# Kernel optimization log

Hardware: AMD Instinct MI355X
Metric: run time of the kernel (lower is better)

Reference implementation:

```python
import jax, jax.numpy as jnp
import numpy as np

DIM = 1024
DIM_QK = 1024
DIM_V = 1024
H = 16
SCALE = 1.0 / (DIM_QK ** 0.5)  # NOTE: module scales by sqrt(dim_qk), not sqrt(head_dim)


def setup_inputs() -> dict:
    key = jax.random.key(0)
    ks = jax.random.split(key, 12)
    B, S = 2, 2048
    q = jax.random.normal(ks[0], (B, S, DIM), jnp.float32)
    k = jax.random.normal(ks[1], (B, S, DIM), jnp.float32)
    v = jax.random.normal(ks[2], (B, S, DIM), jnp.float32)
    mask = jax.random.randint(ks[3], (B, 1, S, S), 0, 2) > 0  # True = masked
    s = 1.0 / np.sqrt(DIM)
    Wq = jax.random.uniform(ks[4], (DIM_QK, DIM), jnp.float32, -s, s)
    bq = jax.random.uniform(ks[5], (DIM_QK,), jnp.float32, -s, s)
    Wk = jax.random.uniform(ks[6], (DIM_QK, DIM), jnp.float32, -s, s)
    bk = jax.random.uniform(ks[7], (DIM_QK,), jnp.float32, -s, s)
    Wv = jax.random.uniform(ks[8], (DIM_V, DIM), jnp.float32, -s, s)
    bv = jax.random.uniform(ks[9], (DIM_V,), jnp.float32, -s, s)
    Wo = jax.random.uniform(ks[10], (DIM_V, DIM), jnp.float32, -s, s)
    bo = jax.random.uniform(ks[11], (DIM_V,), jnp.float32, -s, s)
    return {"q": q, "k": k, "v": v, "mask": mask,
            "Wq": Wq, "bq": bq, "Wk": Wk, "bk": bk,
            "Wv": Wv, "bv": bv, "Wo": Wo, "bo": bo}


def reference(q, k, v, mask, Wq, bq, Wk, bk, Wv, bv, Wo, bo):
    B, Sq, _ = q.shape
    Skv = k.shape[1]
    # projections (torch Linear: x @ W.T + b)
    qh = (q @ Wq.T + bq).reshape(B, Sq, H, DIM_QK // H).transpose(0, 2, 1, 3)   # [B,H,Sq,dk]
    kh = (k @ Wk.T + bk).reshape(B, Skv, H, DIM_QK // H).transpose(0, 2, 1, 3)  # [B,H,Skv,dk]
    vh = (v @ Wv.T + bv).reshape(B, Skv, H, DIM_V // H).transpose(0, 2, 1, 3)   # [B,H,Skv,dv]
    attn = jnp.einsum('bhqd,bhkd->bhqk', qh, kh) * SCALE
    attn = jnp.where(mask, jnp.float32(-1e20), attn)
    attn = jax.nn.softmax(attn, axis=-1)
    # dropout is identity in eval / p=0
    out = jnp.einsum('bhqk,bhkd->bhqd', attn, vh)            # [B,H,Sq,dv]
    out = out.transpose(0, 2, 1, 3).reshape(B, Sq, DIM_V)
    return out @ Wo.T + bo
```

## Files before the change

kernel.cpp:

```cpp
#include <hip/hip_runtime.h>
#include <hip/hip_bf16.h>

typedef __attribute__((ext_vector_type(8))) __bf16 bf16x8;
typedef __attribute__((ext_vector_type(4))) short short4v;
typedef __attribute__((ext_vector_type(4))) float f32x4;
typedef __attribute__((ext_vector_type(4))) unsigned int uint4v;
typedef __attribute__((ext_vector_type(2))) unsigned int uint2v;

#define S_LEN 2048
#define DIM_  1024
#define HDIM  64
#define SCALE2 0.045084441f
#define T_STR 72

#define EXP2F(x) __builtin_amdgcn_exp2f(x)

__device__ __forceinline__ void async_copy16(const void* gp, void* lp) {
  __builtin_amdgcn_global_load_lds(
      (const __attribute__((address_space(1))) unsigned int*)gp,
      (__attribute__((address_space(3))) unsigned int*)lp, 16, 0, 0);
}

__device__ __forceinline__ unsigned f2bf_u(float f) {
  unsigned u = __builtin_bit_cast(unsigned, f);
  return (u + 0x7FFFu + ((u >> 16) & 1u)) >> 16;
}
__device__ __forceinline__ unsigned pack2(float a, float b) {
  return f2bf_u(a) | (f2bf_u(b) << 16);
}
__device__ __forceinline__ unsigned pack2f(float a, float b) {
  unsigned ua = __builtin_bit_cast(unsigned, a) + 0x8000u;
  unsigned ub = __builtin_bit_cast(unsigned, b) + 0x8000u;
  return __builtin_amdgcn_perm(ub, ua, 0x07060302u);
}

__global__ __launch_bounds__(256) void cvt_kernel(
    const float* __restrict__ s0, const float* __restrict__ s1, const float* __restrict__ s2,
    const float* __restrict__ s3, const float* __restrict__ s4, const float* __restrict__ s5,
    const float* __restrict__ s6,
    __hip_bfloat16* __restrict__ d0, __hip_bfloat16* __restrict__ d1, __hip_bfloat16* __restrict__ d2,
    __hip_bfloat16* __restrict__ d3, __hip_bfloat16* __restrict__ d4, __hip_bfloat16* __restrict__ d5,
    __hip_bfloat16* __restrict__ d6)
{
  const float* srcs[7] = {s0, s1, s2, s3, s4, s5, s6};
  __hip_bfloat16* dsts[7] = {d0, d1, d2, d3, d4, d5, d6};
  const int sizes[7] = {4194304, 4194304, 4194304, 1048576, 1048576, 1048576, 1048576};
  int rg = blockIdx.y;
  int base = (blockIdx.x * 256 + threadIdx.x) * 8;
  if (base >= sizes[rg]) return;
  const float* s = srcs[rg] + base;
  f32x4 a = *(const f32x4*)s;
  f32x4 b = *(const f32x4*)(s + 4);
  uint4v o;
  o.x = pack2(a[0], a[1]); o.y = pack2(a[2], a[3]);
  o.z = pack2(b[0], b[1]); o.w = pack2(b[2], b[3]);
  *(uint4v*)(dsts[rg] + base) = o;
}

__global__ __launch_bounds__(256) void maskbits_kernel(
    const int* __restrict__ mask, unsigned long long* __restrict__ bits)
{
  int w = (blockIdx.x * 256 + threadIdx.x) >> 6;
  int lane = threadIdx.x & 63;
  int m = mask[(size_t)w * 64 + lane];
  unsigned long long bal = __ballot(m != 0);
  if (lane == 0) bits[w] = bal;
}

__device__ __forceinline__ void swz(int r, int& m0, int& n0) {
  int g  = r >> 6;
  int yy = (r >> 3) & 7;
  int xl = r & 7;
  m0 = (g * 8 + xl) * 128;
  n0 = yy * 128;
}

__global__ __launch_bounds__(256) void qkv_gemm_kernel(
    const __hip_bfloat16* __restrict__ xq, const __hip_bfloat16* __restrict__ xk,
    const __hip_bfloat16* __restrict__ xv,
    const __hip_bfloat16* __restrict__ Wq, const float* __restrict__ bq,
    const __hip_bfloat16* __restrict__ Wk, const float* __restrict__ bk,
    const __hip_bfloat16* __restrict__ Wv, const float* __restrict__ bv,
    __hip_bfloat16* __restrict__ Q, __hip_bfloat16* __restrict__ Kk,
    __hip_bfloat16* __restrict__ VT)
{
  const __hip_bfloat16 *X, *W; const float* bias;
  if (blockIdx.z == 0)      { X = xq; W = Wq; bias = bq; }
  else if (blockIdx.z == 1) { X = xk; W = Wk; bias = bk; }
  else                      { X = xv; W = Wv; bias = bv; }

  constexpr int K = 1024, N = 1024;
  __shared__ alignas(16) __hip_bfloat16 As[128 * 32];
  __shared__ alignas(16) __hip_bfloat16 Bs[128 * 32];
  const int tid  = threadIdx.x;
  const int lane = tid & 63;
  const int wave = tid >> 6;
  const int t    = lane & 15;
  const int quad = lane >> 4;
  const int wm   = wave >> 1;
  const int wn   = wave & 1;
  int m0, n0;
  swz(blockIdx.x, m0, n0);

  f32x4 acc[4][4] = {};

  for (int k0 = 0; k0 < K; k0 += 32) {
    __syncthreads();
#pragma unroll
    for (int r = 0; r < 2; ++r) {
      int c   = r * 256 + tid;
      int row = c >> 2;
      int col = (c & 3) * 8;
      async_copy16(&X[(size_t)(m0 + row) * K + k0 + col], &As[c * 8]);
      async_copy16(&W[(size_t)(n0 + row) * K + k0 + col], &Bs[c * 8]);
    }
    __syncthreads();
    bf16x8 a[4], b[4];
#pragma unroll
    for (int i = 0; i < 4; ++i)
      a[i] = *(const bf16x8*)&As[(wm * 64 + i * 16 + t) * 32 + quad * 8];
#pragma unroll
    for (int j = 0; j < 4; ++j)
      b[j] = *(const bf16x8*)&Bs[(wn * 64 + j * 16 + t) * 32 + quad * 8];
#pragma unroll
    for (int i = 0; i < 4; ++i)
#pragma unroll
      for (int j = 0; j < 4; ++j)
        acc[i][j] = __builtin_amdgcn_mfma_f32_16x16x32_bf16(a[i], b[j], acc[i][j], 0, 0, 0);
  }

  float bj[4];
#pragma unroll
  for (int j = 0; j < 4; ++j)
    bj[j] = bias[n0 + wn * 64 + j * 16 + t];

  if (blockIdx.z == 2) {
#pragma unroll
    for (int i = 0; i < 4; ++i)
#pragma unroll
      for (int j = 0; j < 4; ++j) {
        int m = m0 + wm * 64 + i * 16 + quad * 4;
        int n = n0 + wn * 64 + j * 16 + t;
        int bb = m >> 11, kv = m & 2047;
        int hh = n >> 6,  dv = n & 63;
        uint2v o;
        o.x = pack2(acc[i][j][0] + bj[j], acc[i][j][1] + bj[j]);
        o.y = pack2(acc[i][j][2] + bj[j], acc[i][j][3] + bj[j]);
        *(uint2v*)&VT[(size_t)(((bb * 16 + hh) * 64) + dv) * 2048 + kv] = o;
      }
  } else {
    const bool isq = (blockIdx.z == 0);
    __hip_bfloat16* Out = isq ? Q : Kk;
    const float sc = isq ? SCALE2 : 1.0f;
#pragma unroll
    for (int i = 0; i < 4; ++i)
#pragma unroll
      for (int j = 0; j < 4; ++j)
#pragma unroll
        for (int r = 0; r < 4; ++r) {
          int m = m0 + wm * 64 + i * 16 + quad * 4 + r;
          int n = n0 + wn * 64 + j * 16 + t;
          Out[(size_t)m * N + n] = __float2bfloat16((acc[i][j][r] + bj[j]) * sc);
        }
  }
}

__global__ __launch_bounds__(256) void proj_gemm_kernel(
    const __hip_bfloat16* __restrict__ X, const __hip_bfloat16* __restrict__ W,
    const float* __restrict__ bias, float* __restrict__ Out)
{
  constexpr int K = 1024, N = 1024;
  __shared__ alignas(16) __hip_bfloat16 As[128 * 32];
  __shared__ alignas(16) __hip_bfloat16 Bs[128 * 32];
  const int tid  = threadIdx.x;
  const int lane = tid & 63;
  const int wave = tid >> 6;
  const int t    = lane & 15;
  const int quad = lane >> 4;
  const int wm   = wave >> 1;
  const int wn   = wave & 1;
  int m0, n0;
  swz(blockIdx.x, m0, n0);

  f32x4 acc[4][4] = {};

  for (int k0 = 0; k0 < K; k0 += 32) {
    __syncthreads();
#pragma unroll
    for (int r = 0; r < 2; ++r) {
      int c   = r * 256 + tid;
      int row = c >> 2;
      int col = (c & 3) * 8;
      async_copy16(&X[(size_t)(m0 + row) * K + k0 + col], &As[c * 8]);
      async_copy16(&W[(size_t)(n0 + row) * K + k0 + col], &Bs[c * 8]);
    }
    __syncthreads();
    bf16x8 a[4], b[4];
#pragma unroll
    for (int i = 0; i < 4; ++i)
      a[i] = *(const bf16x8*)&As[(wm * 64 + i * 16 + t) * 32 + quad * 8];
#pragma unroll
    for (int j = 0; j < 4; ++j)
      b[j] = *(const bf16x8*)&Bs[(wn * 64 + j * 16 + t) * 32 + quad * 8];
#pragma unroll
    for (int i = 0; i < 4; ++i)
#pragma unroll
      for (int j = 0; j < 4; ++j)
        acc[i][j] = __builtin_amdgcn_mfma_f32_16x16x32_bf16(a[i], b[j], acc[i][j], 0, 0, 0);
  }

  float bj[4];
#pragma unroll
  for (int j = 0; j < 4; ++j)
    bj[j] = bias[n0 + wn * 64 + j * 16 + t];
#pragma unroll
  for (int i = 0; i < 4; ++i)
#pragma unroll
    for (int j = 0; j < 4; ++j)
#pragma unroll
      for (int r = 0; r < 4; ++r) {
        int m = m0 + wm * 64 + i * 16 + quad * 4 + r;
        int n = n0 + wn * 64 + j * 16 + t;
        Out[(size_t)m * N + n] = acc[i][j][r] + bj[j];
      }
}

__global__ __launch_bounds__(256) void attn_kernel(
    const __hip_bfloat16* __restrict__ Qb,
    const __hip_bfloat16* __restrict__ Kb,
    const __hip_bfloat16* __restrict__ VT,
    const unsigned long long* __restrict__ mbits,
    __hip_bfloat16* __restrict__ Ob)
{
  const int bid = blockIdx.x;
  const int qt = bid & 31;
  const int h  = (bid >> 5) & 15;
  const int b  = bid >> 9;
  const int qb = qt * 64;

  __shared__ alignas(16) __hip_bfloat16 Qs[64 * T_STR];
  __shared__ alignas(16) __hip_bfloat16 Ks[64 * T_STR];
  __shared__ alignas(16) __hip_bfloat16 Vt[64 * T_STR];

  const int tid  = threadIdx.x;
  const int lane = tid & 63;
  const int wave = tid >> 6;
  const int t    = lane & 15;
  const int quad = lane >> 4;
  const int t7   = t & 7;

#pragma unroll
  for (int r = 0; r < 2; ++r) {
    int c = r * 256 + tid;
    int row = c >> 3, cg = c & 7;
    uint4 raw = *(const uint4*)&Qb[((size_t)(b * S_LEN + qb + row)) * DIM_ + h * HDIM + cg * 8];
    *(uint4*)&Qs[row * T_STR + ((cg ^ (row & 7))) * 8] = raw;
  }
  __syncthreads();

  bf16x8 qf[2];
#pragma unroll
  for (int ks = 0; ks < 2; ++ks)
    qf[ks] = *(const bf16x8*)&Qs[(wave * 16 + t) * T_STR + ((ks * 4 + quad) ^ t7) * 8];

  float lp = 0.f;
  f32x4 o[4] = {};

  const int qg = qb + wave * 16 + t;
  const size_t vtbase = (size_t)((b * 16 + h) * 64) * 2048;
  const size_t mbase = ((size_t)b * S_LEN + qg) * 32;

  for (int kvt = 0; kvt < 32; ++kvt) {
    const int kvb = kvt * 64;
    unsigned long long mw = mbits[mbase + kvt];
    __syncthreads();
#pragma unroll
    for (int r = 0; r < 2; ++r) {
      int c = r * 256 + tid;
      int row = c >> 3, cg = c & 7;
      int sg8 = ((cg ^ (row & 7))) * 8;
      uint4 kraw = *(const uint4*)&Kb[((size_t)(b * S_LEN + kvb + row)) * DIM_ + h * HDIM + cg * 8];
      *(uint4*)&Ks[row * T_STR + sg8] = kraw;
      uint4 vraw = *(const uint4*)&VT[vtbase + (size_t)row * 2048 + kvb + cg * 8];
      *(uint4*)&Vt[row * T_STR + sg8] = vraw;
    }
    __syncthreads();

    f32x4 s4[4];
#pragma unroll
    for (int i = 0; i < 4; ++i) {
      f32x4 z = {};
      bf16x8 a0 = *(const bf16x8*)&Ks[(i * 16 + t) * T_STR + (quad ^ t7) * 8];
      z = __builtin_amdgcn_mfma_f32_16x16x32_bf16(a0, qf[0], z, 0, 0, 0);
      bf16x8 a1 = *(const bf16x8*)&Ks[(i * 16 + t) * T_STR + ((4 + quad) ^ t7) * 8];
      z = __builtin_amdgcn_mfma_f32_16x16x32_bf16(a1, qf[1], z, 0, 0, 0);
      s4[i] = z;
    }

    float e[4][4];
#pragma unroll
    for (int i = 0; i < 4; ++i) {
      unsigned mq = (unsigned)((mw >> (i * 16 + quad * 4)) & 0xFull);
#pragma unroll
      for (int r = 0; r < 4; ++r) {
        float v = ((mq >> r) & 1u) ? -1e20f : s4[i][r];
        float ex = EXP2F(v);
        e[i][r] = ex;
        lp += ex;
      }
    }

    short4v pf[4];
#pragma unroll
    for (int j = 0; j < 4; ++j) {
      uint2v pk;
      pk.x = pack2f(e[j][0], e[j][1]);
      pk.y = pack2f(e[j][2], e[j][3]);
      pf[j] = __builtin_bit_cast(short4v, pk);
    }

#pragma unroll
    for (int j = 0; j < 4; ++j)
#pragma unroll
      for (int n = 0; n < 4; ++n) {
        short4v va = *(const short4v*)&Vt[(n * 16 + t) * T_STR +
                                          (((2 * j + (quad >> 1)) ^ t7) * 8) + (quad & 1) * 4];
        o[n] = __builtin_amdgcn_mfma_f32_16x16x16bf16_1k(va, pf[j], o[n], 0, 0, 0);
      }
  }

  lp += __shfl_xor(lp, 16, 64);
  lp += __shfl_xor(lp, 32, 64);
  float rl = 1.0f / lp;

  __hip_bfloat16* Ts = Qs;
  __syncthreads();
#pragma unroll
  for (int n = 0; n < 4; ++n) {
    uint2v pk;
    pk.x = pack2f(o[n][0] * rl, o[n][1] * rl);
    pk.y = pack2f(o[n][2] * rl, o[n][3] * rl);
    *(uint2v*)&Ts[(wave * 16 + t) * T_STR +
                  (((2 * n + (quad >> 1)) ^ t7) * 8) + (quad & 1) * 4] = pk;
  }
  __syncthreads();
  {
    int row = tid >> 2;
    int g0  = (tid & 3) * 2;
    uint4 x0 = *(const uint4*)&Ts[row * T_STR + ((g0 ^ (row & 7))) * 8];
    uint4 x1 = *(const uint4*)&Ts[row * T_STR + (((g0 + 1) ^ (row & 7))) * 8];
    __hip_bfloat16* dst = &Ob[((size_t)(b * S_LEN + qb + row)) * DIM_ + h * HDIM + g0 * 8];
    *(uint4*)dst = x0;
    *(uint4*)(dst + 8) = x1;
  }
}

extern "C" void kernel_launch(void* const* d_in, const int* in_sizes, int n_in,
                              void* d_out, int out_size, void* d_ws, size_t ws_size,
                              hipStream_t stream) {
  const float* q  = (const float*)d_in[0];
  const float* k  = (const float*)d_in[1];
  const float* v  = (const float*)d_in[2];
  const int*   mk = (const int*)d_in[3];
  const float* Wq = (const float*)d_in[4];
  const float* bq = (const float*)d_in[5];
  const float* Wk = (const float*)d_in[6];
  const float* bk = (const float*)d_in[7];
  const float* Wv = (const float*)d_in[8];
  const float* bv = (const float*)d_in[9];
  const float* Wo = (const float*)d_in[10];
  const float* bo = (const float*)d_in[11];
  float* out = (float*)d_out;

  char* ws = (char*)d_ws;
  const size_t MB = 1024 * 1024;
  __hip_bfloat16* Qb  = (__hip_bfloat16*)(ws);
  __hip_bfloat16* Kb  = (__hip_bfloat16*)(ws + 8  * MB);
  __hip_bfloat16* VTb = (__hip_bfloat16*)(ws + 16 * MB);
  __hip_bfloat16* Ob  = (__hip_bfloat16*)(ws + 24 * MB);
  __hip_bfloat16* xqb = (__hip_bfloat16*)(ws + 32 * MB);
  __hip_bfloat16* xkb = (__hip_bfloat16*)(ws + 40 * MB);
  __hip_bfloat16* xvb = (__hip_bfloat16*)(ws + 48 * MB);
  __hip_bfloat16* Wqb = (__hip_bfloat16*)(ws + 56 * MB);
  __hip_bfloat16* Wkb = (__hip_bfloat16*)(ws + 58 * MB);
  __hip_bfloat16* Wvb = (__hip_bfloat16*)(ws + 60 * MB);
  __hip_bfloat16* Wob = (__hip_bfloat16*)(ws + 62 * MB);
  unsigned long long* mbits = (unsigned long long*)(ws + 64 * MB);

  cvt_kernel<<<dim3(2048, 7), 256, 0, stream>>>(q, k, v, Wq, Wk, Wv, Wo,
                                                xqb, xkb, xvb, Wqb, Wkb, Wvb, Wob);
  maskbits_kernel<<<dim3(32768), 256, 0, stream>>>(mk, mbits);
  qkv_gemm_kernel<<<dim3(256, 1, 3), 256, 0, stream>>>(xqb, xkb, xvb,
                                                       Wqb, bq, Wkb, bk, Wvb, bv,
                                                       Qb, Kb, VTb);
  attn_kernel<<<dim3(1024), 256, 0, stream>>>(Qb, Kb, VTb, mbits, Ob);
  proj_gemm_kernel<<<dim3(256), 256, 0, stream>>>(Ob, Wob, bo, out);
}
```

Baseline: 314.3 us.

## Double KV tile to 128 and replace XOR swizzle with padded LDS strides

The attention kernel now processes 128 keys per iteration instead of 64, which halves the number of loop iterations and barrier pairs. The XOR-swizzled LDS layout is replaced by plain padded row strides (80 for Q/K, 136 for V^T). The aim is to cut synchronisation and address arithmetic overhead. In exchange it uses more LDS and registers per block, which may reduce occupancy, and the padded layout may cause different bank conflicts.

Result: slower. 356.8 us (+13.5%).

```diff
diff --git a/kernel.cpp b/kernel.cpp
--- a/kernel.cpp
+++ b/kernel.cpp
@@ -11,7 +11,8 @@
 #define DIM_  1024
 #define HDIM  64
 #define SCALE2 0.045084441f
-#define T_STR 72
+#define QK_STR 80
+#define VT_STR 136
 
 #define EXP2F(x) __builtin_amdgcn_exp2f(x)
 
@@ -238,30 +239,29 @@
   const int b  = bid >> 9;
   const int qb = qt * 64;
 
-  __shared__ alignas(16) __hip_bfloat16 Qs[64 * T_STR];
-  __shared__ alignas(16) __hip_bfloat16 Ks[64 * T_STR];
-  __shared__ alignas(16) __hip_bfloat16 Vt[64 * T_STR];
+  __shared__ alignas(16) __hip_bfloat16 Qs[64 * QK_STR];
+  __shared__ alignas(16) __hip_bfloat16 Ks[128 * QK_STR];
+  __shared__ alignas(16) __hip_bfloat16 Vt[64 * VT_STR];
 
   const int tid  = threadIdx.x;
   const int lane = tid & 63;
   const int wave = tid >> 6;
   const int t    = lane & 15;
   const int quad = lane >> 4;
-  const int t7   = t & 7;
 
 #pragma unroll
   for (int r = 0; r < 2; ++r) {
     int c = r * 256 + tid;
-    int row = c >> 3, cg = c & 7;
-    uint4 raw = *(const uint4*)&Qb[((size_t)(b * S_LEN + qb + row)) * DIM_ + h * HDIM + cg * 8];
-    *(uint4*)&Qs[row * T_STR + ((cg ^ (row & 7))) * 8] = raw;
+    int row = c >> 3, d0 = (c & 7) * 8;
+    uint4 raw = *(const uint4*)&Qb[((size_t)(b * S_LEN + qb + row)) * DIM_ + h * HDIM + d0];
+    *(uint4*)&Qs[row * QK_STR + d0] = raw;
   }
   __syncthreads();
 
   bf16x8 qf[2];
 #pragma unroll
   for (int ks = 0; ks < 2; ++ks)
-    qf[ks] = *(const bf16x8*)&Qs[(wave * 16 + t) * T_STR + ((ks * 4 + quad) ^ t7) * 8];
+    qf[ks] = *(const bf16x8*)&Qs[(wave * 16 + t) * QK_STR + ks * 32 + quad * 8];
 
   float lp = 0.f;
   f32x4 o[4] = {};
@@ -270,49 +270,49 @@
   const size_t vtbase = (size_t)((b * 16 + h) * 64) * 2048;
   const size_t mbase = ((size_t)b * S_LEN + qg) * 32;
 
-  for (int kvt = 0; kvt < 32; ++kvt) {
-    const int kvb = kvt * 64;
-    unsigned long long mw = mbits[mbase + kvt];
-    __syncthreads();
-#pragma unroll
-    for (int r = 0; r < 2; ++r) {
+  for (int kvt = 0; kvt < 16; ++kvt) {
+    const int kvb = kvt * 128;
+    unsigned long long mw0 = mbits[mbase + kvt * 2];
+    unsigned long long mw1 = mbits[mbase + kvt * 2 + 1];
+    __syncthreads();
+#pragma unroll
+    for (int r = 0; r < 4; ++r) {
       int c = r * 256 + tid;
-      int row = c >> 3, cg = c & 7;
-      int sg8 = ((cg ^ (row & 7))) * 8;
-      uint4 kraw = *(const uint4*)&Kb[((size_t)(b * S_LEN + kvb + row)) * DIM_ + h * HDIM + cg * 8];
-      *(uint4*)&Ks[row * T_STR + sg8] = kraw;
-      uint4 vraw = *(const uint4*)&VT[vtbase + (size_t)row * 2048 + kvb + cg * 8];
-      *(uint4*)&Vt[row * T_STR + sg8] = vraw;
-    }
-    __syncthreads();
-
-    f32x4 s4[4];
-#pragma unroll
-    for (int i = 0; i < 4; ++i) {
+      int row = c >> 3, d0 = (c & 7) * 8;
+      uint4 kraw = *(const uint4*)&Kb[((size_t)(b * S_LEN + kvb + row)) * DIM_ + h * HDIM + d0];
+      *(uint4*)&Ks[row * QK_STR + d0] = kraw;
+    }
+#pragma unroll
+    for (int r = 0; r < 4; ++r) {
+      int c = r * 256 + tid;
+      int row = c >> 4, cg = (c & 15) * 8;
+      uint4 vraw = *(const uint4*)&VT[vtbase + (size_t)row * 2048 + kvb + cg];
+      *(uint4*)&Vt[row * VT_STR + cg] = vraw;
+    }
+    __syncthreads();
+
+    float e[8][4];
+#pragma unroll
+    for (int i = 0; i < 8; ++i) {
       f32x4 z = {};
-      bf16x8 a0 = *(const bf16x8*)&Ks[(i * 16 + t) * T_STR + (quad ^ t7) * 8];
+      bf16x8 a0 = *(const bf16x8*)&Ks[(i * 16 + t) * QK_STR + quad * 8];
       z = __builtin_amdgcn_mfma_f32_16x16x32_bf16(a0, qf[0], z, 0, 0, 0);
-      bf16x8 a1 = *(const bf16x8*)&Ks[(i * 16 + t) * T_STR + ((4 + quad) ^ t7) * 8];
+      bf16x8 a1 = *(const bf16x8*)&Ks[(i * 16 + t) * QK_STR + 32 + quad * 8];
       z = __builtin_amdgcn_mfma_f32_16x16x32_bf16(a1, qf[1], z, 0, 0, 0);
-      s4[i] = z;
-    }
-
-    float e[4][4];
-#pragma unroll
-    for (int i = 0; i < 4; ++i) {
-      unsigned mq = (unsigned)((mw >> (i * 16 + quad * 4)) & 0xFull);
+      unsigned long long mw = (i < 4) ? mw0 : mw1;
+      unsigned mq = (unsigned)((mw >> ((i & 3) * 16 + quad * 4)) & 0xFull);
 #pragma unroll
       for (int r = 0; r < 4; ++r) {
-        float v = ((mq >> r) & 1u) ? -1e20f : s4[i][r];
+        float v = ((mq >> r) & 1u) ? -1e20f : z[r];
         float ex = EXP2F(v);
         e[i][r] = ex;
         lp += ex;
       }
     }
 
-    short4v pf[4];
-#pragma unroll
-    for (int j = 0; j < 4; ++j) {
+    short4v pf[8];
+#pragma unroll
+    for (int j = 0; j < 8; ++j) {
       uint2v pk;
       pk.x = pack2f(e[j][0], e[j][1]);
       pk.y = pack2f(e[j][2], e[j][3]);
@@ -320,11 +320,10 @@
     }
 
 #pragma unroll
-    for (int j = 0; j < 4; ++j)
+    for (int j = 0; j < 8; ++j)
 #pragma unroll
       for (int n = 0; n < 4; ++n) {
-        short4v va = *(const short4v*)&Vt[(n * 16 + t) * T_STR +
-                                          (((2 * j + (quad >> 1)) ^ t7) * 8) + (quad & 1) * 4];
+        short4v va = *(const short4v*)&Vt[(n * 16 + t) * VT_STR + j * 16 + quad * 4];
         o[n] = __builtin_amdgcn_mfma_f32_16x16x16bf16_1k(va, pf[j], o[n], 0, 0, 0);
       }
   }
@@ -340,16 +339,15 @@
     uint2v pk;
     pk.x = pack2f(o[n][0] * rl, o[n][1] * rl);
     pk.y = pack2f(o[n][2] * rl, o[n][3] * rl);
-    *(uint2v*)&Ts[(wave * 16 + t) * T_STR +
-                  (((2 * n + (quad >> 1)) ^ t7) * 8) + (quad & 1) * 4] = pk;
+    *(uint2v*)&Ts[(wave * 16 + t) * QK_STR + n * 16 + quad * 4] = pk;
   }
   __syncthreads();
   {
     int row = tid >> 2;
-    int g0  = (tid & 3) * 2;
-    uint4 x0 = *(const uint4*)&Ts[row * T_STR + ((g0 ^ (row & 7))) * 8];
-    uint4 x1 = *(const uint4*)&Ts[row * T_STR + (((g0 + 1) ^ (row & 7))) * 8];
-    __hip_bfloat16* dst = &Ob[((size_t)(b * S_LEN + qb + row)) * DIM_ + h * HDIM + g0 * 8];
+    int d0  = (tid & 3) * 16;
+    uint4 x0 = *(const uint4*)&Ts[row * QK_STR + d0];
+    uint4 x1 = *(const uint4*)&Ts[row * QK_STR + d0 + 8];
+    __hip_bfloat16* dst = &Ob[((size_t)(b * S_LEN + qb + row)) * DIM_ + h * HDIM + d0];
     *(uint4*)dst = x0;
     *(uint4*)(dst + 8) = x1;
   }
```
